# Performance work log

Measured on AMD Instinct MI355X. Metric: run time of the kernel, lower is better.

## Reference

```python
import jax, jax.numpy as jnp
import numpy as np

N_NODES = 50000
N_EDGES = 800000
DIM_A = 96
DIM_V = 64
R0 = 2.0
LEAK = 0.1
EPS = 1e-12


def radial_encode_8(r_vec, r0):
    # Soft one-hot (tent) radial basis over 8 bins on [0, r0].
    r = jnp.linalg.norm(r_vec, axis=-1)                      # [E]
    u = r * (8.0 / r0)
    k = jnp.arange(8, dtype=r.dtype)
    return jax.nn.relu(1.0 - jnp.abs(u[..., None] - k))      # [E, 8]


def tens_sigmoid_rank1(x):
    # Equivariant norm-squashing of a rank-1 tensor: direction kept, norm -> tanh(norm).
    n = jnp.linalg.norm(x, axis=-1, keepdims=True)
    return x * (jnp.tanh(n) / jnp.maximum(n, EPS))


def leaky(x):
    return jnp.where(x >= 0, x, LEAK * x)


def setup_inputs() -> dict:
    key = jax.random.key(0)
    ks = jax.random.split(key, 8)
    s = lambda k, sh, fan: jax.random.normal(k, sh, jnp.float32) / np.float32(np.sqrt(fan))
    r_ij = jax.random.normal(ks[0], (N_EDGES, 3), jnp.float32)
    src = jax.random.randint(ks[1], (N_EDGES,), 0, N_NODES, jnp.int32)
    return {
        "r_ij": r_ij,
        "w0": s(ks[2], (DIM_A, 8), 8),   "b0": jnp.zeros((DIM_A,), jnp.float32),
        "w1": s(ks[3], (DIM_A, DIM_A), DIM_A), "b1": jnp.zeros((DIM_A,), jnp.float32),
        "w2": s(ks[4], (DIM_A, DIM_A), DIM_A), "b2": jnp.zeros((DIM_A,), jnp.float32),
        "w3": s(ks[5], (DIM_A, DIM_A), DIM_A),
        "wv": s(ks[6], (DIM_V, DIM_A), DIM_A),
        "src": src,
    }


def reference(r_ij, w0, b0, w1, b1, w2, b2, w3, wv, src):
    # Per-edge radial MLP: Linear(8,da) -> [Linear, LeakyReLU, Linear, LeakyReLU, Linear(no bias)]
    enc = radial_encode_8(r_ij, R0)                          # [E, 8]
    h = enc @ w0.T + b0                                      # [E, da]
    h = leaky(h @ w1.T + b1)
    h = leaky(h @ w2.T + b2)
    rad = h @ w3.T                                           # [E, da]
    rv = tens_sigmoid_rank1(r_ij * (7.0 / R0))               # [E, 3]
    phi_v = rad[:, :, None] * rv[:, None, :]                 # [E, da, 3]
    A_a = jax.ops.segment_sum(rad, src, num_segments=N_NODES)     # [N, da]
    A_v = jax.ops.segment_sum(phi_v, src, num_segments=N_NODES)   # [N, da, 3]
    out_v = jnp.einsum('va,nac->nvc', wv, A_v)               # [N, dv, 3]
    return (A_a, out_v)
```

## Files before the change

kernel.cpp:

```cpp
#include <hip/hip_runtime.h>
#include <math.h>

typedef float f32x4 __attribute__((ext_vector_type(4)));
typedef short s16x8 __attribute__((ext_vector_type(8)));

__device__ __forceinline__ unsigned short f2bf(float f) {
    unsigned u = __builtin_bit_cast(unsigned, f);
    u += 0x7fffu + ((u >> 16) & 1u);
    return (unsigned short)(u >> 16);
}

__device__ __forceinline__ int xcd_swizzle(int b, int nwg) {
    int q = nwg >> 3, r = nwg & 7;
    int xcd = b & 7, slot = b >> 3;
    int base = (xcd < r) ? xcd * (q + 1) : r * (q + 1) + (xcd - r) * q;
    return base + slot;
}

#define PACK_TOT 36864

__global__ __launch_bounds__(256) void pack_weights_k(
    const float* __restrict__ w0, const float* __restrict__ w1,
    const float* __restrict__ w2, const float* __restrict__ w3,
    const float* __restrict__ wv, unsigned short* __restrict__ dst)
{
    int idx = blockIdx.x * 256 + threadIdx.x;
    if (idx >= PACK_TOT) return;
    const float* W; int inF, ntiles, off;
    if (idx < 3072)       { W = w0; inF = 8;  ntiles = 6; off = 0; }
    else if (idx < 12288) { W = w1; inF = 96; ntiles = 6; off = 3072; }
    else if (idx < 21504) { W = w2; inF = 96; ntiles = 6; off = 12288; }
    else if (idx < 30720) { W = w3; inF = 96; ntiles = 6; off = 21504; }
    else                  { W = wv; inF = 96; ntiles = 4; off = 30720; }
    int r  = idx - off;
    int fi = r >> 9;
    int wi = r & 511;
    int l = wi >> 3, j = wi & 7;
    int kt = fi / ntiles, nt = fi - kt * ntiles;
    int n = nt * 16 + (l & 15);
    int k = kt * 32 + ((l >> 4) << 3) + j;
    float v = (k < inF) ? W[n * inF + k] : 0.0f;
    dst[idx] = f2bf(v);
}

__global__ __launch_bounds__(256) void hist_k(const int* __restrict__ src,
                                              int* __restrict__ counts, int E)
{
    int e = blockIdx.x * 256 + threadIdx.x;
    if (e < E) atomicAdd(&counts[src[e]], 1);
}

__global__ __launch_bounds__(256) void scan1_k(const int* __restrict__ counts,
                                               int* __restrict__ cursor,
                                               int* __restrict__ bsum, int N)
{
    __shared__ int wsum_s[4];
    int b = blockIdx.x, t = threadIdx.x, lane = t & 63, wid = t >> 6;
    int i0 = b * 2048 + t * 8;
    int v[8]; int s = 0;
    #pragma unroll
    for (int j = 0; j < 8; j++) { int i = i0 + j; v[j] = (i < N) ? counts[i] : 0; s += v[j]; }
    int inc = s;
    #pragma unroll
    for (int d = 1; d < 64; d <<= 1) { int o = __shfl_up(inc, d, 64); if (lane >= d) inc += o; }
    if (lane == 63) wsum_s[wid] = inc;
    __syncthreads();
    int wb = 0;
    for (int k = 0; k < wid; k++) wb += wsum_s[k];
    int run = wb + inc - s;
    #pragma unroll
    for (int j = 0; j < 8; j++) { int i = i0 + j; if (i < N) cursor[i] = run; run += v[j]; }
    if (t == 255) bsum[b] = wb + inc;
}

__global__ __launch_bounds__(64) void scan2_k(int* __restrict__ bsum, int nb)
{
    int lane = threadIdx.x;
    int v = (lane < nb) ? bsum[lane] : 0;
    int inc = v;
    #pragma unroll
    for (int d = 1; d < 64; d <<= 1) { int o = __shfl_up(inc, d, 64); if (lane >= d) inc += o; }
    if (lane < nb) bsum[lane] = inc - v;
}

__global__ __launch_bounds__(256) void scatter_k(const int* __restrict__ src,
                                                 const float* __restrict__ r_ij,
                                                 const int* __restrict__ bsum,
                                                 int* __restrict__ cursor,
                                                 int* __restrict__ order,
                                                 int* __restrict__ srcs,
                                                 float4* __restrict__ rsrt,
                                                 int use_rsrt, int E)
{
    int e = blockIdx.x * 256 + threadIdx.x;
    if (e < E) {
        int s = src[e];
        int p = bsum[s >> 11] + atomicAdd(&cursor[s], 1);
        if (use_rsrt) {
            rsrt[p] = make_float4(r_ij[3*e], r_ij[3*e+1], r_ij[3*e+2], __int_as_float(s));
        } else {
            order[p] = e;
            srcs[p] = s;
        }
    }
}

__global__ __launch_bounds__(256, 4) void edge_kernel(
    const float* __restrict__ r_ij,
    const int* __restrict__ order, const int* __restrict__ srcs,
    const float4* __restrict__ rsrt, int use_rsrt,
    const unsigned short* __restrict__ wp,
    const float* __restrict__ b0, const float* __restrict__ b1, const float* __restrict__ b2,
    float* __restrict__ A_a, float* __restrict__ Ov, int E)
{
    __shared__ unsigned short h_s[16896];
    __shared__ unsigned short rvb_s[3 * 128];
    __shared__ unsigned char  segid_s[128];
    __shared__ int  segnode_s[128];
    __shared__ int  src_s[128];
    __shared__ int  nseg_s;

    const int tid = threadIdx.x;
    const int w  = tid >> 6;
    const int l  = tid & 63;
    const int e0 = xcd_swizzle(blockIdx.x, gridDim.x) * 128;
    const int lr = l & 15;
    const int lg = l >> 4;
    const int mbase = w * 32;

    if (l < 32) {
        const int ml = mbase + l;
        const int pos = e0 + ml;
        float x = 0.f, y = 0.f, z = 0.f; int s = -1;
        if (pos < E) {
            if (use_rsrt) {
                float4 v4 = rsrt[pos];
                x = v4.x; y = v4.y; z = v4.z; s = __float_as_int(v4.w);
            } else {
                int e = order[pos];
                s = srcs[pos];
                x = r_ij[3*e]; y = r_ij[3*e+1]; z = r_ij[3*e+2];
            }
        }
        float r = sqrtf(x*x + y*y + z*z);
        float u = r * 4.0f;
        s16x8 ev;
        #pragma unroll
        for (int k = 0; k < 8; k++) {
            float t = fmaxf(1.0f - fabsf(u - (float)k), 0.0f);
            ev[k] = (short)f2bf((s >= 0) ? t : 0.0f);
        }
        *(s16x8*)&h_s[ml * 104 + 96] = ev;
        float nn = 3.5f * r;
        float sc = (s >= 0) ? (3.5f * tanhf(nn) / fmaxf(nn, 1e-12f)) : 0.0f;
        rvb_s[0*128 + ml] = f2bf(x * sc);
        rvb_s[1*128 + ml] = f2bf(y * sc);
        rvb_s[2*128 + ml] = f2bf(z * sc);
        src_s[ml] = s;
    }
    __syncthreads();

    if (w == 0) {
        int i = l;
        int sA = src_s[i];
        bool fA = (i == 0) || (sA != src_s[i - 1]);
        unsigned long long mA = __ballot(fA);
        unsigned long long maskA = (~0ull) >> (63 - i);
        int incA = (int)__popcll(mA & maskA);
        segid_s[i] = (unsigned char)(incA - 1);
        if (fA) segnode_s[incA - 1] = sA;
        int totA = (int)__popcll(mA);
        int jrow = 64 + i;
        int sB = src_s[jrow];
        bool fB = (sB != src_s[jrow - 1]);
        unsigned long long mB = __ballot(fB);
        int incB = (int)__popcll(mB & maskA);
        segid_s[jrow] = (unsigned char)(totA + incB - 1);
        if (fB) segnode_s[totA + incB - 1] = sB;
        if (i == 63) nseg_s = totA + (int)__popcll(mB);
    }

    float b0v[6], b1v[6], b2v[6];
    #pragma unroll
    for (int nt = 0; nt < 6; nt++) {
        b0v[nt] = b0[nt*16 + lr];
        b1v[nt] = b1[nt*16 + lr];
        b2v[nt] = b2[nt*16 + lr];
    }

    {
        s16x8 A0[2];
        #pragma unroll
        for (int mf = 0; mf < 2; mf++) {
            s16x8 a = {0,0,0,0,0,0,0,0};
            if (l < 16) a = *(const s16x8*)&h_s[(mbase + mf*16 + lr) * 104 + 96];
            A0[mf] = a;
        }
        f32x4 acc[2][6];
        #pragma unroll
        for (int nt = 0; nt < 6; nt++) {
            s16x8 B = *(const s16x8*)&wp[nt * 512 + l * 8];
            f32x4 bi = {b0v[nt], b0v[nt], b0v[nt], b0v[nt]};
            acc[0][nt] = __builtin_amdgcn_mfma_f32_16x16x32_bf16(A0[0], B, bi, 0, 0, 0);
            acc[1][nt] = __builtin_amdgcn_mfma_f32_16x16x32_bf16(A0[1], B, bi, 0, 0, 0);
        }
        #pragma unroll
        for (int mf = 0; mf < 2; mf++)
        #pragma unroll
        for (int nt = 0; nt < 6; nt++)
        #pragma unroll
        for (int j = 0; j < 4; j++)
            h_s[(mbase + mf*16 + lg*4 + j) * 104 + nt*16 + lr] = f2bf(acc[mf][nt][j]);
    }

    #pragma unroll
    for (int li = 0; li < 2; li++) {
        const int poff = 3072 + li * 9216;
        s16x8 A[2][3];
        #pragma unroll
        for (int mf = 0; mf < 2; mf++)
        #pragma unroll
        for (int kt = 0; kt < 3; kt++)
            A[mf][kt] = *(const s16x8*)&h_s[(mbase + mf*16 + lr) * 104 + kt*32 + lg*8];
        f32x4 a2[2][6];
        #pragma unroll
        for (int nt = 0; nt < 6; nt++) {
            float bb = (li == 0) ? b1v[nt] : b2v[nt];
            f32x4 bi = {bb, bb, bb, bb};
            a2[0][nt] = bi; a2[1][nt] = bi;
        }
        #pragma unroll
        for (int nt = 0; nt < 6; nt++)
        #pragma unroll
        for (int kt = 0; kt < 3; kt++) {
            s16x8 B = *(const s16x8*)&wp[poff + (kt*6 + nt) * 512 + l * 8];
            a2[0][nt] = __builtin_amdgcn_mfma_f32_16x16x32_bf16(A[0][kt], B, a2[0][nt], 0, 0, 0);
            a2[1][nt] = __builtin_amdgcn_mfma_f32_16x16x32_bf16(A[1][kt], B, a2[1][nt], 0, 0, 0);
        }
        #pragma unroll
        for (int mf = 0; mf < 2; mf++)
        #pragma unroll
        for (int nt = 0; nt < 6; nt++)
        #pragma unroll
        for (int j = 0; j < 4; j++) {
            float v = a2[mf][nt][j];
            v = fmaxf(v, 0.1f * v);
            h_s[(mbase + mf*16 + lg*4 + j) * 104 + nt*16 + lr] = f2bf(v);
        }
    }

    uint2 radp[2][6];
    {
        s16x8 A[2][3];
        #pragma unroll
        for (int mf = 0; mf < 2; mf++)
        #pragma unroll
        for (int kt = 0; kt < 3; kt++)
            A[mf][kt] = *(const s16x8*)&h_s[(mbase + mf*16 + lr) * 104 + kt*32 + lg*8];
        f32x4 rad[2][6] = {};
        #pragma unroll
        for (int nt = 0; nt < 6; nt++)
        #pragma unroll
        for (int kt = 0; kt < 3; kt++) {
            s16x8 B = *(const s16x8*)&wp[21504 + (kt*6 + nt) * 512 + l * 8];
            rad[0][nt] = __builtin_amdgcn_mfma_f32_16x16x32_bf16(A[0][kt], B, rad[0][nt], 0, 0, 0);
            rad[1][nt] = __builtin_amdgcn_mfma_f32_16x16x32_bf16(A[1][kt], B, rad[1][nt], 0, 0, 0);
        }
        #pragma unroll
        for (int mf = 0; mf < 2; mf++)
        #pragma unroll
        for (int nt = 0; nt < 6; nt++) {
            unsigned short q0 = f2bf(rad[mf][nt][0]);
            unsigned short q1 = f2bf(rad[mf][nt][1]);
            unsigned short q2 = f2bf(rad[mf][nt][2]);
            unsigned short q3 = f2bf(rad[mf][nt][3]);
            radp[mf][nt].x = (unsigned)q0 | ((unsigned)q1 << 16);
            radp[mf][nt].y = (unsigned)q2 | ((unsigned)q3 << 16);
        }
    }

    __syncthreads();

    #pragma unroll
    for (int mf = 0; mf < 2; mf++)
    #pragma unroll
    for (int nt = 0; nt < 6; nt++)
        *(uint2*)&h_s[(w*6 + nt) * 512 + ((2*mf + (lg>>1))*16 + lr) * 8 + (lg&1)*4] = radp[mf][nt];

    __syncthreads();

    const int nseg = nseg_s;
    if (w == 0) {
        for (int st = 0; st * 16 < nseg; ++st) {
            const int target = st * 16 + lr;
            f32x4 acc[6] = {};
            #pragma unroll
            for (int kt = 0; kt < 4; kt++) {
                uint2 sid8 = *(const uint2*)&segid_s[kt*32 + 8*lg];
                s16x8 af;
                #pragma unroll
                for (int j = 0; j < 8; j++) {
                    unsigned word = (j < 4) ? sid8.x : sid8.y;
                    int sid = (word >> (8 * (j & 3))) & 255;
                    af[j] = (short)((sid == target) ? 0x3F80 : 0);
                }
                #pragma unroll
                for (int nt = 0; nt < 6; nt++) {
                    s16x8 B = *(const s16x8*)&h_s[(kt*6 + nt) * 512 + l * 8];
                    acc[nt] = __builtin_amdgcn_mfma_f32_16x16x32_bf16(af, B, acc[nt], 0, 0, 0);
                }
            }
            #pragma unroll
            for (int nt = 0; nt < 6; nt++)
            #pragma unroll
            for (int j = 0; j < 4; j++) {
                int g = st*16 + 4*lg + j;
                if (g < nseg) {
                    int node = segnode_s[g];
                    if (node >= 0)
                        unsafeAtomicAdd(&A_a[node*96 + nt*16 + lr], acc[nt][j]);
                }
            }
        }
    } else {
        const int c = w - 1;
        const int scb = 12288 + (w - 1) * 1536;
        for (int st = 0; st * 16 < nseg; ++st) {
            const int target = st * 16 + lr;
            f32x4 acc6[6] = {};
            #pragma unroll
            for (int kt = 0; kt < 4; kt++) {
                uint2 sid8 = *(const uint2*)&segid_s[kt*32 + 8*lg];
                s16x8 rv8 = *(const s16x8*)&rvb_s[c*128 + kt*32 + 8*lg];
                s16x8 af;
                #pragma unroll
                for (int j = 0; j < 8; j++) {
                    unsigned word = (j < 4) ? sid8.x : sid8.y;
                    int sid = (word >> (8 * (j & 3))) & 255;
                    af[j] = (sid == target) ? rv8[j] : (short)0;
                }
                #pragma unroll
                for (int nt = 0; nt < 6; nt++) {
                    s16x8 B = *(const s16x8*)&h_s[(kt*6 + nt) * 512 + l * 8];
                    acc6[nt] = __builtin_amdgcn_mfma_f32_16x16x32_bf16(af, B, acc6[nt], 0, 0, 0);
                }
            }
            #pragma unroll
            for (int nt = 0; nt < 6; nt++) {
                int ktf = nt >> 1;
                int lane2 = ((nt & 1) * 2 + (lr >> 3)) * 16 + 4*lg;
                int a0 = scb + ktf*512 + lane2*8 + (lr & 7);
                h_s[a0]      = f2bf(acc6[nt][0]);
                h_s[a0 + 8]  = f2bf(acc6[nt][1]);
                h_s[a0 + 16] = f2bf(acc6[nt][2]);
                h_s[a0 + 24] = f2bf(acc6[nt][3]);
            }
            s16x8 As[3];
            #pragma unroll
            for (int ktf = 0; ktf < 3; ktf++)
                As[ktf] = *(const s16x8*)&h_s[scb + ktf*512 + l*8];
            f32x4 acc2[4] = {};
            #pragma unroll
            for (int vt = 0; vt < 4; vt++)
            #pragma unroll
            for (int ktf = 0; ktf < 3; ktf++) {
                s16x8 B = *(const s16x8*)&wp[30720 + (ktf*4 + vt) * 512 + l * 8];
                acc2[vt] = __builtin_amdgcn_mfma_f32_16x16x32_bf16(As[ktf], B, acc2[vt], 0, 0, 0);
            }
            #pragma unroll
            for (int vt = 0; vt < 4; vt++)
            #pragma unroll
            for (int j = 0; j < 4; j++) {
                int g = st*16 + 4*lg + j;
                if (g < nseg) {
                    int node = segnode_s[g];
                    if (node >= 0)
                        unsafeAtomicAdd(&Ov[node*192 + (vt*16 + lr)*3 + c], acc2[vt][j]);
                }
            }
        }
    }
}

extern "C" void kernel_launch(void* const* d_in, const int* in_sizes, int n_in,
                              void* d_out, int out_size, void* d_ws, size_t ws_size,
                              hipStream_t stream)
{
    const float* r_ij = (const float*)d_in[0];
    const float* w0   = (const float*)d_in[1];
    const float* b0   = (const float*)d_in[2];
    const float* w1   = (const float*)d_in[3];
    const float* b1   = (const float*)d_in[4];
    const float* w2   = (const float*)d_in[5];
    const float* b2   = (const float*)d_in[6];
    const float* w3   = (const float*)d_in[7];
    const float* wv   = (const float*)d_in[8];
    const int*   src  = (const int*)d_in[9];
    const int E = in_sizes[0] / 3;
    const int N = out_size / 288;
    float* A_a = (float*)d_out;
    float* Ov  = A_a + (size_t)N * 96;

    char* wsb = (char*)d_ws;
    unsigned short* wp = (unsigned short*)wsb;
    size_t off = 73728;
    int* counts = (int*)(wsb + off);  off += (((size_t)N*4 + 127) & ~127ull);
    int* cursor = (int*)(wsb + off);  off += (((size_t)N*4 + 127) & ~127ull);
    int* bsum   = (int*)(wsb + off);  off += 256;
    size_t need_rsrt = off + (size_t)E * 16;
    int use_rsrt = (need_rsrt <= ws_size) ? 1 : 0;
    float4* rsrt = (float4*)(wsb + off);
    int* order   = (int*)(wsb + off);
    int* srcs    = (int*)(wsb + off + (((size_t)E*4 + 127) & ~127ull));

    const int nb = (N + 2047) / 2048;

    hipMemsetAsync(d_out, 0, (size_t)out_size * sizeof(float), stream);
    hipMemsetAsync(counts, 0, (size_t)N * 4, stream);

    pack_weights_k<<<(PACK_TOT + 255) / 256, 256, 0, stream>>>(w0, w1, w2, w3, wv, wp);
    hist_k<<<(E + 255) / 256, 256, 0, stream>>>(src, counts, E);
    scan1_k<<<nb, 256, 0, stream>>>(counts, cursor, bsum, N);
    scan2_k<<<1, 64, 0, stream>>>(bsum, nb);
    scatter_k<<<(E + 255) / 256, 256, 0, stream>>>(src, r_ij, bsum, cursor,
                                                   order, srcs, rsrt, use_rsrt, E);
    edge_kernel<<<(E + 127) / 128, 256, 0, stream>>>(r_ij, order, srcs, rsrt, use_rsrt,
                                                     wp, b0, b1, b2, A_a, Ov, E);
}
```

Before: 271.8 us.

## Fold block-sum scan into scatter kernel and relax edge kernel occupancy bound

Removes the separate single-wave scan2 kernel launch. Each scatter block now redundantly scans the block sums into shared memory before placing its edges. The block-sum scan also gains a loop, so it is no longer limited to 64 blocks, and the bsum workspace slot grows to match. Separately, the edge kernel's launch bound drops from 4 to 3 waves-per-SIMD blocks, allowing more registers per thread at the cost of occupancy.

```diff
diff --git a/kernel.cpp b/kernel.cpp
--- a/kernel.cpp
+++ b/kernel.cpp
@@ -73,16 +73,6 @@
     if (t == 255) bsum[b] = wb + inc;
 }
 
-__global__ __launch_bounds__(64) void scan2_k(int* __restrict__ bsum, int nb)
-{
-    int lane = threadIdx.x;
-    int v = (lane < nb) ? bsum[lane] : 0;
-    int inc = v;
-    #pragma unroll
-    for (int d = 1; d < 64; d <<= 1) { int o = __shfl_up(inc, d, 64); if (lane >= d) inc += o; }
-    if (lane < nb) bsum[lane] = inc - v;
-}
-
 __global__ __launch_bounds__(256) void scatter_k(const int* __restrict__ src,
                                                  const float* __restrict__ r_ij,
                                                  const int* __restrict__ bsum,
@@ -90,12 +80,30 @@
                                                  int* __restrict__ order,
                                                  int* __restrict__ srcs,
                                                  float4* __restrict__ rsrt,
-                                                 int use_rsrt, int E)
-{
-    int e = blockIdx.x * 256 + threadIdx.x;
+                                                 int use_rsrt, int nb, int E)
+{
+    __shared__ int pre_s[256];
+    int t = threadIdx.x;
+    if (t < 64) {
+        int carry = 0;
+        for (int base = 0; base < nb; base += 64) {
+            int i = base + t;
+            int v = (i < nb) ? bsum[i] : 0;
+            int inc = v;
+            #pragma unroll
+            for (int d = 1; d < 64; d <<= 1) {
+                int o = __shfl_up(inc, d, 64);
+                if (t >= d) inc += o;
+            }
+            if (i < nb) pre_s[i] = carry + inc - v;
+            carry += __shfl(inc, 63);
+        }
+    }
+    __syncthreads();
+    int e = blockIdx.x * 256 + t;
     if (e < E) {
         int s = src[e];
-        int p = bsum[s >> 11] + atomicAdd(&cursor[s], 1);
+        int p = pre_s[s >> 11] + atomicAdd(&cursor[s], 1);
         if (use_rsrt) {
             rsrt[p] = make_float4(r_ij[3*e], r_ij[3*e+1], r_ij[3*e+2], __int_as_float(s));
         } else {
@@ -105,7 +113,7 @@
     }
 }
 
-__global__ __launch_bounds__(256, 4) void edge_kernel(
+__global__ __launch_bounds__(256, 3) void edge_kernel(
     const float* __restrict__ r_ij,
     const int* __restrict__ order, const int* __restrict__ srcs,
     const float4* __restrict__ rsrt, int use_rsrt,
@@ -406,7 +414,7 @@
     size_t off = 73728;
     int* counts = (int*)(wsb + off);  off += (((size_t)N*4 + 127) & ~127ull);
     int* cursor = (int*)(wsb + off);  off += (((size_t)N*4 + 127) & ~127ull);
-    int* bsum   = (int*)(wsb + off);  off += 256;
+    int* bsum   = (int*)(wsb + off);  off += 1024;
     size_t need_rsrt = off + (size_t)E * 16;
     int use_rsrt = (need_rsrt <= ws_size) ? 1 : 0;
     float4* rsrt = (float4*)(wsb + off);
@@ -421,9 +429,8 @@
     pack_weights_k<<<(PACK_TOT + 255) / 256, 256, 0, stream>>>(w0, w1, w2, w3, wv, wp);
     hist_k<<<(E + 255) / 256, 256, 0, stream>>>(src, counts, E);
     scan1_k<<<nb, 256, 0, stream>>>(counts, cursor, bsum, N);
-    scan2_k<<<1, 64, 0, stream>>>(bsum, nb);
     scatter_k<<<(E + 255) / 256, 256, 0, stream>>>(src, r_ij, bsum, cursor,
-                                                   order, srcs, rsrt, use_rsrt, E);
+                                                   order, srcs, rsrt, use_rsrt, nb, E);
     edge_kernel<<<(E + 127) / 128, 256, 0, stream>>>(r_ij, order, srcs, rsrt, use_rsrt,
                                                      wp, b0, b1, b2, A_a, Ov, E);
 }
```

Result: faster. 255.4 us (-6.0%).
